# Kernel tuning notes

Hardware: AMD Instinct MI355X
Metric: run time of the kernel (lower is better)

## Reference

```python
import jax, jax.numpy as jnp
import numpy as np

N_TOKEN = 267735
D = 512           # d_embed == d_proj
DIV = 4
CUTS = [0, 20000, 40000, 200000, 267735]  # cutoff_ends
N_TOKENS_BATCH = 1024  # len*bsz


def setup_inputs() -> dict:
    key = jax.random.key(0)
    ks = jax.random.split(key, 16)
    inp = {}
    inp["hidden"] = jax.random.normal(ks[0], (N_TOKENS_BATCH, D), jnp.float32)
    inp["target"] = jax.random.randint(ks[1], (N_TOKENS_BATCH,), 0, N_TOKEN)
    d_embs = [D // DIV ** i for i in range(4)]          # 512, 128, 32, 8
    sizes = [CUTS[i + 1] - CUTS[i] for i in range(4)]   # 20000, 20000, 160000, 67735
    for i in range(4):
        inp[f"W{i}"] = jax.random.normal(ks[2 + 3 * i], (sizes[i], d_embs[i]), jnp.float32) * (d_embs[i] ** -0.5)
        inp[f"b{i}"] = jax.random.normal(ks[3 + 3 * i], (sizes[i],), jnp.float32) * 0.01
        inp[f"proj{i}"] = jax.random.normal(ks[4 + 3 * i], (D, d_embs[i]), jnp.float32) * (D ** -0.5)
    inp["cluster_weight"] = jax.random.normal(ks[14], (3, D), jnp.float32) * (D ** -0.5)
    inp["cluster_bias"] = jax.random.normal(ks[15], (3,), jnp.float32) * 0.01
    return inp


def reference(hidden, target, W0, b0, proj0, W1, b1, proj1, W2, b2, proj2, W3, b3, proj3, cluster_weight, cluster_bias):
    n = jnp.arange(target.shape[0])
    # head = shortlist vocab + one logit per tail cluster
    head_w = jnp.concatenate([W0, cluster_weight], axis=0)   # [20003, D]
    head_b = jnp.concatenate([b0, cluster_bias], axis=0)     # [20003]
    head_logit = (hidden @ proj0) @ head_w.T + head_b        # einsum('bd,de,ev->bv')
    head_lp = jax.nn.log_softmax(head_logit, axis=-1)        # [N, 20003]
    head_size = head_lp.shape[1]
    # cluster id per token (0 = shortlist, 1..3 = tails)
    cid = ((target >= CUTS[1]).astype(jnp.int32)
           + (target >= CUTS[2]).astype(jnp.int32)
           + (target >= CUTS[3]).astype(jnp.int32))
    # shortlist: nll = -head_logprob[n, target]
    nll = -head_lp[n, jnp.clip(target, 0, CUTS[1] - 1)]
    for i, (Wi, bi, pi) in enumerate([(W1, b1, proj1), (W2, b2, proj2), (W3, b3, proj3)], start=1):
        l, r = CUTS[i], CUTS[i + 1]
        tail_lp = jax.nn.log_softmax((hidden @ pi) @ Wi.T + bi, axis=-1)  # [N, r-l]
        rel = jnp.clip(target - l, 0, r - l - 1)
        # faithful to original: head column indexed as head_logprob[:, -i]
        lp_i = head_lp[:, head_size - i] + tail_lp[n, rel]
        nll = jnp.where(cid == i, -lp_i, nll)
    return nll
```

## Files before the change

kernel.cpp:

```cpp
#include <hip/hip_runtime.h>

typedef short s16x8 __attribute__((ext_vector_type(8)));
typedef unsigned short u16x8 __attribute__((ext_vector_type(8)));
typedef float f32x4 __attribute__((ext_vector_type(4)));
typedef unsigned short ushort;

#define NTOK 1024
#define DHID 512

#define VH   20003
#define KH   512
#define NCH_H 80
#define TPC_H 16
#define VH_PAD 20480

#define V1   20000
#define K1   128
#define NCH_1 80
#define TPC_1 16
#define V1_PAD 20480

#define V2   160000
#define K2   32
#define NCH_2 128
#define TPC_2 80
#define V2_PAD 163840

#define V3   67735
#define K3   32
#define NCH_3 67
#define TPC_3 64
#define V3_PAD 68608

#define PAD_BIAS (-1e30f)

#define OFF_HW   0UL
#define OFF_W1   (OFF_HW  + (unsigned long)VH_PAD*KH*2)
#define OFF_W2   (OFF_W1  + (unsigned long)V1_PAD*K1*2)
#define OFF_W3   (OFF_W2  + (unsigned long)V2_PAD*K2*2)
#define OFF_HID  (OFF_W3  + (unsigned long)V3_PAD*K3*2)
#define OFF_PT0  (OFF_HID + (unsigned long)NTOK*DHID*2)
#define OFF_PT1  (OFF_PT0 + (unsigned long)512*DHID*2)
#define OFF_PT2  (OFF_PT1 + (unsigned long)128*DHID*2)
#define OFF_PT3  (OFF_PT2 + (unsigned long)32*DHID*2)
#define OFF_H0   (OFF_PT3 + (unsigned long)32*DHID*2)
#define OFF_H1   (OFF_H0  + (unsigned long)NTOK*512*2)
#define OFF_H2   (OFF_H1  + (unsigned long)NTOK*128*2)
#define OFF_H3   (OFF_H2  + (unsigned long)NTOK*32*2)
#define OFF_HB   (OFF_H3  + (unsigned long)NTOK*32*2)
#define OFF_B1   (OFF_HB  + (unsigned long)VH_PAD*4)
#define OFF_B2   (OFF_B1  + (unsigned long)V1_PAD*4)
#define OFF_B3   (OFF_B2  + (unsigned long)V2_PAD*4)
#define OFF_SH   (OFF_B3  + (unsigned long)V3_PAD*4)
#define OFF_S1   (OFF_SH  + (unsigned long)NTOK*NCH_H*4)
#define OFF_S2   (OFF_S1  + (unsigned long)NTOK*NCH_1*4)
#define OFF_S3   (OFF_S2  + (unsigned long)NTOK*NCH_2*4)

__device__ __forceinline__ ushort f2bf(float f) {
    union { float f; unsigned u; } x; x.f = f;
    unsigned r = x.u + 0x7fffu + ((x.u >> 16) & 1u);
    return (ushort)(r >> 16);
}
__device__ __forceinline__ float bf2f(ushort h) {
    union { unsigned u; float f; } x; x.u = ((unsigned)h) << 16;
    return x.f;
}
__device__ __forceinline__ f32x4 mfma_bf16(s16x8 a, s16x8 b, f32x4 c) {
    return __builtin_amdgcn_mfma_f32_16x16x32_bf16(a, b, c, 0, 0, 0);
}
__device__ __forceinline__ void ld8(const float* p, float* v) {
    float4 a = *(const float4*)p, b = *(const float4*)(p + 4);
    v[0]=a.x; v[1]=a.y; v[2]=a.z; v[3]=a.w; v[4]=b.x; v[5]=b.y; v[6]=b.z; v[7]=b.w;
}

#define WB_HW  20480L
#define WB_W1  5120L
#define WB_W2  10240L
#define WB_W3  4288L
#define WB_HID 1024L
#define WB_PT0 512L
#define WB_PT1 128L
#define WB_PT2 32L
#define WB_PT3 32L
#define WB_TOTAL (WB_HW+WB_W1+WB_W2+WB_W3+WB_HID+WB_PT0+WB_PT1+WB_PT2+WB_PT3)

__global__ __launch_bounds__(256) void prep_wswz(
    const float* __restrict__ hidden,
    const float* __restrict__ W0, const float* __restrict__ cw,
    const float* __restrict__ W1, const float* __restrict__ W2, const float* __restrict__ W3,
    const float* __restrict__ p0, const float* __restrict__ p1,
    const float* __restrict__ p2, const float* __restrict__ p3,
    ushort* __restrict__ hw, ushort* __restrict__ ow1,
    ushort* __restrict__ ow2, ushort* __restrict__ ow3,
    ushort* __restrict__ hid,
    ushort* __restrict__ pT0, ushort* __restrict__ pT1,
    ushort* __restrict__ pT2, ushort* __restrict__ pT3)
{
    int lane = threadIdx.x & 63;
    int r = lane & 15, quad = lane >> 4;
    long wb0 = (long)blockIdx.x * 4 + (threadIdx.x >> 6);
    long nw = (long)gridDim.x * 4;
    for (long wb = wb0; wb < WB_TOTAL; wb += nw) {
        long b = wb;
        float vals[8];
        #pragma unroll
        for (int j = 0; j < 8; ++j) vals[j] = 0.f;
        ushort* dst;
        if (b < WB_HW) {
            long tile = b >> 4, ks = b & 15;
            long v = tile * 16 + r, k = ks * 32 + quad * 8;
            if (v < 20000)      ld8(W0 + v * 512 + k, vals);
            else if (v < VH)    ld8(cw + (v - 20000) * 512 + k, vals);
            dst = hw + b * 512 + (long)lane * 8;
        } else if ((b -= WB_HW) < WB_W1) {
            long tile = b >> 2, ks = b & 3;
            long v = tile * 16 + r, k = ks * 32 + quad * 8;
            if (v < V1) ld8(W1 + v * 128 + k, vals);
            dst = ow1 + b * 512 + (long)lane * 8;
        } else if ((b -= WB_W1) < WB_W2) {
            long v = b * 16 + r;
            if (v < V2) ld8(W2 + v * 32 + quad * 8, vals);
            dst = ow2 + b * 512 + (long)lane * 8;
        } else if ((b -= WB_W2) < WB_W3) {
            long v = b * 16 + r;
            if (v < V3 && quad == 0) ld8(W3 + v * 8, vals);
            dst = ow3 + b * 512 + (long)lane * 8;
        } else if ((b -= WB_W3) < WB_HID) {
            long tile = b >> 4, ks = b & 15;
            long v = tile * 16 + r, k = ks * 32 + quad * 8;
            ld8(hidden + v * 512 + k, vals);
            dst = hid + b * 512 + (long)lane * 8;
        } else if ((b -= WB_HID) < WB_PT0) {
            long tile = b >> 4, ks = b & 15;
            long c = tile * 16 + r, k = ks * 32 + quad * 8;
            #pragma unroll
            for (int j = 0; j < 8; ++j) vals[j] = p0[(k + j) * 512 + c];
            dst = pT0 + b * 512 + (long)lane * 8;
        } else if ((b -= WB_PT0) < WB_PT1) {
            long tile = b >> 4, ks = b & 15;
            long c = tile * 16 + r, k = ks * 32 + quad * 8;
            #pragma unroll
            for (int j = 0; j < 8; ++j) vals[j] = p1[(k + j) * 128 + c];
            dst = pT1 + b * 512 + (long)lane * 8;
        } else if ((b -= WB_PT1) < WB_PT2) {
            long tile = b >> 4, ks = b & 15;
            long c = tile * 16 + r, k = ks * 32 + quad * 8;
            #pragma unroll
            for (int j = 0; j < 8; ++j) vals[j] = p2[(k + j) * 32 + c];
            dst = pT2 + b * 512 + (long)lane * 8;
        } else {
            b -= WB_PT2;
            long tile = b >> 4, ks = b & 15;
            long c = tile * 16 + r, k = ks * 32 + quad * 8;
            if (c < 8) {
                #pragma unroll
                for (int j = 0; j < 8; ++j) vals[j] = p3[(k + j) * 8 + c];
            }
            dst = pT3 + b * 512 + (long)lane * 8;
        }
        u16x8 o;
        #pragma unroll
        for (int j = 0; j < 8; ++j) o[j] = f2bf(vals[j]);
        *(u16x8*)dst = o;
    }
}

#define E_HB  ((long)VH_PAD)
#define E_B1  ((long)V1_PAD)
#define E_B2  ((long)V2_PAD)
#define E_B3  ((long)V3_PAD)
#define E_BIAS (E_HB+E_B1+E_B2+E_B3)

__global__ __launch_bounds__(256) void prep_bias(
    const float* __restrict__ b0, const float* __restrict__ b1,
    const float* __restrict__ b2, const float* __restrict__ b3,
    const float* __restrict__ cb,
    float* __restrict__ hbp, float* __restrict__ ob1,
    float* __restrict__ ob2, float* __restrict__ ob3)
{
    long stride = (long)gridDim.x * blockDim.x;
    for (long i = (long)blockIdx.x * blockDim.x + threadIdx.x; i < E_BIAS; i += stride) {
        long j = i;
        if (j < E_HB) {
            hbp[j] = (j < 20000) ? b0[j] : (j < VH) ? cb[j - 20000] : PAD_BIAS;
        } else if ((j -= E_HB) < E_B1) {
            ob1[j] = (j < V1) ? b1[j] : PAD_BIAS;
        } else if ((j -= E_B1) < E_B2) {
            ob2[j] = (j < V2) ? b2[j] : PAD_BIAS;
        } else { j -= E_B2;
            ob3[j] = (j < V3) ? b3[j] : PAD_BIAS;
        }
    }
}

__global__ __launch_bounds__(256) void gemm_h(
    const ushort* __restrict__ A, const ushort* __restrict__ Bt,
    ushort* __restrict__ Hout, int dpad)
{
    int wave = threadIdx.x >> 6, lane = threadIdx.x & 63;
    int quad = lane >> 4, colid = lane & 15;
    int m_tile = blockIdx.x * 4 + wave;
    int c_tile = blockIdx.y;
    const ushort* Ab = A + ((long)m_tile * 16) * 512 + lane * 8;
    const ushort* Bb = Bt + ((long)c_tile * 16) * 512 + lane * 8;
    f32x4 acc = {0.f, 0.f, 0.f, 0.f};
    #pragma unroll
    for (int ks = 0; ks < 16; ++ks) {
        s16x8 a = *(const s16x8*)(Ab + ks * 512);
        s16x8 b = *(const s16x8*)(Bb + ks * 512);
        acc = mfma_bf16(a, b, acc);
    }
    int KBo = dpad >> 5;
    int col = c_tile * 16 + colid;
    int ks_o = col >> 5, q_o = (col >> 3) & 3, j_o = col & 7;
    #pragma unroll
    for (int r = 0; r < 4; ++r) {
        int rm = quad * 4 + r;
        Hout[((long)m_tile * KBo + ks_o) * 512 + (q_o * 16 + rm) * 8 + j_o] = f2bf(acc[r]);
    }
}

template<int K, int U>
__global__ __launch_bounds__(256, 4) void fused_lse_t(
    const ushort* __restrict__ A, const ushort* __restrict__ W,
    const float* __restrict__ bias, float* __restrict__ part_s,
    int tpc, int n_chunks)
{
    constexpr int KB = K / 32;
    int wave = threadIdx.x >> 6, lane = threadIdx.x & 63;
    int quad = lane >> 4, colid = lane & 15;
    int m_tile = blockIdx.x * 4 + wave;
    int t0 = blockIdx.y * tpc;
    const ushort* Ab = A + ((long)m_tile * KB) * 512 + lane * 8;
    float s_acc[4] = {0.f, 0.f, 0.f, 0.f};

    for (int vt = 0; vt < tpc; vt += U) {
        int tile0 = t0 + vt;
        const ushort* Wb = W + ((long)tile0 * KB) * 512 + lane * 8;
        f32x4 acc[U];
        #pragma unroll
        for (int u = 0; u < U; ++u) acc[u] = (f32x4){0.f, 0.f, 0.f, 0.f};
        #pragma unroll 4
        for (int ks = 0; ks < KB; ++ks) {
            s16x8 a = *(const s16x8*)(Ab + ks * 512);
            #pragma unroll
            for (int u = 0; u < U; ++u) {
                s16x8 b = *(const s16x8*)(Wb + ((long)u * KB + ks) * 512);
                acc[u] = mfma_bf16(a, b, acc[u]);
            }
        }
        #pragma unroll
        for (int u = 0; u < U; ++u) {
            float bval = bias[(tile0 + u) * 16 + colid];
            #pragma unroll
            for (int r = 0; r < 4; ++r)
                s_acc[r] += __expf(acc[u][r] + bval);
        }
    }
    #pragma unroll
    for (int r = 0; r < 4; ++r) {
        float v = s_acc[r];
        v += __shfl_xor(v, 1);
        v += __shfl_xor(v, 2);
        v += __shfl_xor(v, 4);
        v += __shfl_xor(v, 8);
        s_acc[r] = v;
    }
    if (colid == 0) {
        #pragma unroll
        for (int r = 0; r < 4; ++r) {
            int m = m_tile * 16 + quad * 4 + r;
            part_s[(long)m * n_chunks + blockIdx.y] = s_acc[r];
        }
    }
}

__device__ __forceinline__ float swz_dot(const ushort* __restrict__ H, int m,
                                         const ushort* __restrict__ Wm, long vrow,
                                         int K, int lane)
{
    float d = 0.f;
    if (lane * 8 < K) {
        int ks = lane >> 2, q = lane & 3;
        int KB = K >> 5;
        const ushort* hp = H + ((long)(m >> 4) * KB + ks) * 512 + (q * 16 + (m & 15)) * 8;
        const ushort* wp = Wm + ((vrow >> 4) * KB + ks) * 512 + (q * 16 + (int)(vrow & 15)) * 8;
        #pragma unroll
        for (int j = 0; j < 8; ++j) d += bf2f(hp[j]) * bf2f(wp[j]);
    }
    d += __shfl_xor(d, 1);  d += __shfl_xor(d, 2);  d += __shfl_xor(d, 4);
    d += __shfl_xor(d, 8);  d += __shfl_xor(d, 16); d += __shfl_xor(d, 32);
    return d;
}

__global__ __launch_bounds__(256) void finalize_kernel(
    const int* __restrict__ target,
    const ushort* __restrict__ H0, const ushort* __restrict__ hw,
    const float* __restrict__ hbp, const float* __restrict__ sH,
    const ushort* __restrict__ H1, const ushort* __restrict__ w1,
    const float* __restrict__ b1p, const float* __restrict__ s1,
    const ushort* __restrict__ H2, const ushort* __restrict__ w2,
    const float* __restrict__ b2p, const float* __restrict__ s2,
    const ushort* __restrict__ H3, const ushort* __restrict__ w3,
    const float* __restrict__ b3p, const float* __restrict__ s3,
    float* __restrict__ out)
{
    int wave = threadIdx.x >> 6, lane = threadIdx.x & 63;
    int m = blockIdx.x * 4 + wave;
    int t = target[m];
    int cid = (t >= 20000) + (t >= 40000) + (t >= 200000);

    float s = 0.f;
    for (int i = lane; i < NCH_H; i += 64) s += sH[(long)m * NCH_H + i];
    s += __shfl_xor(s, 1);  s += __shfl_xor(s, 2);  s += __shfl_xor(s, 4);
    s += __shfl_xor(s, 8);  s += __shfl_xor(s, 16); s += __shfl_xor(s, 32);
    float lse_h = __logf(s);

    int hc = (cid == 0) ? t : (20003 - cid);
    float d = swz_dot(H0, m, hw, hc, 512, lane);
    float nll = lse_h - (d + hbp[hc]);

    if (cid > 0) {
        const ushort *Hi, *Wi; const float *bi, *si; int K, nc, l;
        if (cid == 1)      { Hi = H1; Wi = w1; bi = b1p; si = s1; K = 128; nc = NCH_1; l = 20000; }
        else if (cid == 2) { Hi = H2; Wi = w2; bi = b2p; si = s2; K = 32;  nc = NCH_2; l = 40000; }
        else               { Hi = H3; Wi = w3; bi = b3p; si = s3; K = 32;  nc = NCH_3; l = 200000; }
        int rel = t - l;
        float ts = 0.f;
        for (int i = lane; i < nc; i += 64) ts += si[(long)m * nc + i];
        ts += __shfl_xor(ts, 1);  ts += __shfl_xor(ts, 2);  ts += __shfl_xor(ts, 4);
        ts += __shfl_xor(ts, 8);  ts += __shfl_xor(ts, 16); ts += __shfl_xor(ts, 32);
        float lse_t = __logf(ts);
        float dt = swz_dot(Hi, m, Wi, rel, K, lane);
        nll += lse_t - (dt + bi[rel]);
    }
    if (lane == 0) out[m] = nll;
}

extern "C" void kernel_launch(void* const* d_in, const int* in_sizes, int n_in,
                              void* d_out, int out_size, void* d_ws, size_t ws_size,
                              hipStream_t stream) {
    const float* hidden = (const float*)d_in[0];
    const int*   target = (const int*)d_in[1];
    const float* W0 = (const float*)d_in[2];
    const float* b0 = (const float*)d_in[3];
    const float* p0 = (const float*)d_in[4];
    const float* W1 = (const float*)d_in[5];
    const float* b1 = (const float*)d_in[6];
    const float* p1 = (const float*)d_in[7];
    const float* W2 = (const float*)d_in[8];
    const float* b2 = (const float*)d_in[9];
    const float* p2 = (const float*)d_in[10];
    const float* W3 = (const float*)d_in[11];
    const float* b3 = (const float*)d_in[12];
    const float* p3 = (const float*)d_in[13];
    const float* cw = (const float*)d_in[14];
    const float* cb = (const float*)d_in[15];

    char* ws = (char*)d_ws;
    ushort* hw  = (ushort*)(ws + OFF_HW);
    ushort* ow1 = (ushort*)(ws + OFF_W1);
    ushort* ow2 = (ushort*)(ws + OFF_W2);
    ushort* ow3 = (ushort*)(ws + OFF_W3);
    ushort* hid = (ushort*)(ws + OFF_HID);
    ushort* pT0 = (ushort*)(ws + OFF_PT0);
    ushort* pT1 = (ushort*)(ws + OFF_PT1);
    ushort* pT2 = (ushort*)(ws + OFF_PT2);
    ushort* pT3 = (ushort*)(ws + OFF_PT3);
    ushort* H0  = (ushort*)(ws + OFF_H0);
    ushort* H1  = (ushort*)(ws + OFF_H1);
    ushort* H2  = (ushort*)(ws + OFF_H2);
    ushort* H3  = (ushort*)(ws + OFF_H3);
    float* hbp = (float*)(ws + OFF_HB);
    float* b1p = (float*)(ws + OFF_B1);
    float* b2p = (float*)(ws + OFF_B2);
    float* b3p = (float*)(ws + OFF_B3);
    float* sH  = (float*)(ws + OFF_SH);
    float* s1  = (float*)(ws + OFF_S1);
    float* s2  = (float*)(ws + OFF_S2);
    float* s3  = (float*)(ws + OFF_S3);

    prep_wswz<<<10464, 256, 0, stream>>>(hidden, W0, cw, W1, W2, W3,
                                         p0, p1, p2, p3,
                                         hw, ow1, ow2, ow3, hid, pT0, pT1, pT2, pT3);
    prep_bias<<<1072, 256, 0, stream>>>(b0, b1, b2, b3, cb, hbp, b1p, b2p, b3p);

    gemm_h<<<dim3(NTOK / 64, 512 / 16), 256, 0, stream>>>(hid, pT0, H0, 512);
    gemm_h<<<dim3(NTOK / 64, 128 / 16), 256, 0, stream>>>(hid, pT1, H1, 128);
    gemm_h<<<dim3(NTOK / 64, 32 / 16),  256, 0, stream>>>(hid, pT2, H2, 32);
    gemm_h<<<dim3(NTOK / 64, 32 / 16),  256, 0, stream>>>(hid, pT3, H3, 32);

    fused_lse_t<KH, 8><<<dim3(NTOK / 64, NCH_H), 256, 0, stream>>>(H0, hw,  hbp, sH, TPC_H, NCH_H);
    fused_lse_t<K1, 8><<<dim3(NTOK / 64, NCH_1), 256, 0, stream>>>(H1, ow1, b1p, s1, TPC_1, NCH_1);
    fused_lse_t<K2, 8><<<dim3(NTOK / 64, NCH_2), 256, 0, stream>>>(H2, ow2, b2p, s2, TPC_2, NCH_2);
    fused_lse_t<K3, 8><<<dim3(NTOK / 64, NCH_3), 256, 0, stream>>>(H3, ow3, b3p, s3, TPC_3, NCH_3);

    finalize_kernel<<<NTOK / 4, 256, 0, stream>>>(target,
        H0, hw, hbp, sH, H1, ow1, b1p, s1, H2, ow2, b2p, s2, H3, ow3, b3p, s3,
        (float*)d_out);
}
```

Baseline: 277.8 us.

## Register-block fused LSE kernel over four row tiles per wave to reuse W loads

The fused log-sum-exp kernel now has each single-wave block compute four 16-row token tiles against the same vocabulary tiles, so each W fragment loaded from memory feeds four MFMAs instead of one. For small K the A fragments are hoisted into registers for the whole chunk. Vocabulary chunk counts are doubled so the grid stays large despite the smaller 64-thread blocks, and the unroll factor drops to 4 for the tail clusters. The cost is higher register pressure, which may lower occupancy, plus twice as many partial sums for finalize to reduce.

```diff
diff --git a/kernel.cpp b/kernel.cpp
--- a/kernel.cpp
+++ b/kernel.cpp
@@ -10,26 +10,26 @@
 
 #define VH   20003
 #define KH   512
-#define NCH_H 80
-#define TPC_H 16
+#define NCH_H 160
+#define TPC_H 8
 #define VH_PAD 20480
 
 #define V1   20000
 #define K1   128
-#define NCH_1 80
-#define TPC_1 16
+#define NCH_1 160
+#define TPC_1 8
 #define V1_PAD 20480
 
 #define V2   160000
 #define K2   32
-#define NCH_2 128
-#define TPC_2 80
+#define NCH_2 256
+#define TPC_2 40
 #define V2_PAD 163840
 
 #define V3   67735
 #define K3   32
-#define NCH_3 67
-#define TPC_3 64
+#define NCH_3 134
+#define TPC_3 32
 #define V3_PAD 68608
 
 #define PAD_BIAS (-1e30f)
@@ -220,58 +220,90 @@
     }
 }
 
-template<int K, int U>
-__global__ __launch_bounds__(256, 4) void fused_lse_t(
+template<int K, int U, int M>
+__global__ __launch_bounds__(64) void fused_lse_t(
     const ushort* __restrict__ A, const ushort* __restrict__ W,
     const float* __restrict__ bias, float* __restrict__ part_s,
     int tpc, int n_chunks)
 {
     constexpr int KB = K / 32;
-    int wave = threadIdx.x >> 6, lane = threadIdx.x & 63;
+    constexpr bool HOIST = (KB <= 4);
+    int lane = threadIdx.x & 63;
     int quad = lane >> 4, colid = lane & 15;
-    int m_tile = blockIdx.x * 4 + wave;
-    int t0 = blockIdx.y * tpc;
-    const ushort* Ab = A + ((long)m_tile * KB) * 512 + lane * 8;
-    float s_acc[4] = {0.f, 0.f, 0.f, 0.f};
+    int mt0 = blockIdx.x * M;
+    int chunk = blockIdx.y;
+    int t0 = chunk * tpc;
+    const ushort* Ab = A + (long)mt0 * KB * 512 + lane * 8;
+
+    float s_acc[M][4];
+    #pragma unroll
+    for (int t = 0; t < M; ++t)
+        #pragma unroll
+        for (int r = 0; r < 4; ++r) s_acc[t][r] = 0.f;
+
+    s16x8 af[M][HOIST ? KB : 1];
+    if constexpr (HOIST) {
+        #pragma unroll
+        for (int t = 0; t < M; ++t)
+            #pragma unroll
+            for (int ks = 0; ks < KB; ++ks)
+                af[t][ks] = *(const s16x8*)(Ab + ((long)t * KB + ks) * 512);
+    }
 
     for (int vt = 0; vt < tpc; vt += U) {
-        int tile0 = t0 + vt;
-        const ushort* Wb = W + ((long)tile0 * KB) * 512 + lane * 8;
-        f32x4 acc[U];
-        #pragma unroll
-        for (int u = 0; u < U; ++u) acc[u] = (f32x4){0.f, 0.f, 0.f, 0.f};
-        #pragma unroll 4
+        const ushort* Wb = W + ((long)(t0 + vt) * KB) * 512 + lane * 8;
+        f32x4 acc[M][U];
+        #pragma unroll
+        for (int t = 0; t < M; ++t)
+            #pragma unroll
+            for (int u = 0; u < U; ++u) acc[t][u] = (f32x4){0.f, 0.f, 0.f, 0.f};
+        #pragma unroll
         for (int ks = 0; ks < KB; ++ks) {
-            s16x8 a = *(const s16x8*)(Ab + ks * 512);
-            #pragma unroll
-            for (int u = 0; u < U; ++u) {
-                s16x8 b = *(const s16x8*)(Wb + ((long)u * KB + ks) * 512);
-                acc[u] = mfma_bf16(a, b, acc[u]);
+            s16x8 b[U];
+            #pragma unroll
+            for (int u = 0; u < U; ++u)
+                b[u] = *(const s16x8*)(Wb + ((long)u * KB + ks) * 512);
+            s16x8 a[M];
+            #pragma unroll
+            for (int t = 0; t < M; ++t) {
+                if constexpr (HOIST) a[t] = af[t][ks];
+                else a[t] = *(const s16x8*)(Ab + ((long)t * KB + ks) * 512);
             }
+            #pragma unroll
+            for (int t = 0; t < M; ++t)
+                #pragma unroll
+                for (int u = 0; u < U; ++u)
+                    acc[t][u] = mfma_bf16(a[t], b[u], acc[t][u]);
         }
         #pragma unroll
         for (int u = 0; u < U; ++u) {
-            float bval = bias[(tile0 + u) * 16 + colid];
-            #pragma unroll
-            for (int r = 0; r < 4; ++r)
-                s_acc[r] += __expf(acc[u][r] + bval);
+            float bval = bias[(t0 + vt + u) * 16 + colid];
+            #pragma unroll
+            for (int t = 0; t < M; ++t)
+                #pragma unroll
+                for (int r = 0; r < 4; ++r)
+                    s_acc[t][r] += __expf(acc[t][u][r] + bval);
         }
     }
     #pragma unroll
-    for (int r = 0; r < 4; ++r) {
-        float v = s_acc[r];
-        v += __shfl_xor(v, 1);
-        v += __shfl_xor(v, 2);
-        v += __shfl_xor(v, 4);
-        v += __shfl_xor(v, 8);
-        s_acc[r] = v;
-    }
+    for (int t = 0; t < M; ++t)
+        #pragma unroll
+        for (int r = 0; r < 4; ++r) {
+            float v = s_acc[t][r];
+            v += __shfl_xor(v, 1);
+            v += __shfl_xor(v, 2);
+            v += __shfl_xor(v, 4);
+            v += __shfl_xor(v, 8);
+            s_acc[t][r] = v;
+        }
     if (colid == 0) {
         #pragma unroll
-        for (int r = 0; r < 4; ++r) {
-            int m = m_tile * 16 + quad * 4 + r;
-            part_s[(long)m * n_chunks + blockIdx.y] = s_acc[r];
-        }
+        for (int t = 0; t < M; ++t)
+            #pragma unroll
+            for (int r = 0; r < 4; ++r) {
+                int m = (mt0 + t) * 16 + quad * 4 + r;
+                part_s[(long)m * n_chunks + chunk] = s_acc[t][r];
+            }
     }
 }
 
@@ -390,10 +422,10 @@
     gemm_h<<<dim3(NTOK / 64, 32 / 16),  256, 0, stream>>>(hid, pT2, H2, 32);
     gemm_h<<<dim3(NTOK / 64, 32 / 16),  256, 0, stream>>>(hid, pT3, H3, 32);
 
-    fused_lse_t<KH, 8><<<dim3(NTOK / 64, NCH_H), 256, 0, stream>>>(H0, hw,  hbp, sH, TPC_H, NCH_H);
-    fused_lse_t<K1, 8><<<dim3(NTOK / 64, NCH_1), 256, 0, stream>>>(H1, ow1, b1p, s1, TPC_1, NCH_1);
-    fused_lse_t<K2, 8><<<dim3(NTOK / 64, NCH_2), 256, 0, stream>>>(H2, ow2, b2p, s2, TPC_2, NCH_2);
-    fused_lse_t<K3, 8><<<dim3(NTOK / 64, NCH_3), 256, 0, stream>>>(H3, ow3, b3p, s3, TPC_3, NCH_3);
+    fused_lse_t<KH, 8, 4><<<dim3(16, NCH_H), 64, 0, stream>>>(H0, hw,  hbp, sH, TPC_H, NCH_H);
+    fused_lse_t<K1, 4, 4><<<dim3(16, NCH_1), 64, 0, stream>>>(H1, ow1, b1p, s1, TPC_1, NCH_1);
+    fused_lse_t<K2, 4, 4><<<dim3(16, NCH_2), 64, 0, stream>>>(H2, ow2, b2p, s2, TPC_2, NCH_2);
+    fused_lse_t<K3, 4, 4><<<dim3(16, NCH_3), 64, 0, stream>>>(H3, ow3, b3p, s3, TPC_3, NCH_3);
 
     finalize_kernel<<<NTOK / 4, 256, 0, stream>>>(target,
         H0, hw, hbp, sH, H1, ow1, b1p, s1, H2, ow2, b2p, s2, H3, ow3, b3p, s3,
```

Result: slower. 372.2 us (+34.0%).

## Stage vocab weight tiles in LDS shared across waves in LSE kernels

Applied to the files above, without the earlier changes.

The fused log-sum-exp kernels now cooperatively load each group of 8 weight tiles into shared memory once per block, and all four waves (each owning a different token tile) read those tiles from LDS. Previously each wave fetched the same weight tiles from global memory on its own. Chunk counts are doubled and tiles per chunk halved to raise grid parallelism. The cost is two barriers per k-slice and LDS pressure, and the occupancy hint was dropped from the launch bounds.

```diff
diff --git a/kernel.cpp b/kernel.cpp
--- a/kernel.cpp
+++ b/kernel.cpp
@@ -10,26 +10,26 @@
 
 #define VH   20003
 #define KH   512
-#define NCH_H 80
-#define TPC_H 16
+#define NCH_H 160
+#define TPC_H 8
 #define VH_PAD 20480
 
 #define V1   20000
 #define K1   128
-#define NCH_1 80
-#define TPC_1 16
+#define NCH_1 160
+#define TPC_1 8
 #define V1_PAD 20480
 
 #define V2   160000
 #define K2   32
-#define NCH_2 128
-#define TPC_2 80
+#define NCH_2 256
+#define TPC_2 40
 #define V2_PAD 163840
 
 #define V3   67735
 #define K3   32
-#define NCH_3 67
-#define TPC_3 64
+#define NCH_3 134
+#define TPC_3 32
 #define V3_PAD 68608
 
 #define PAD_BIAS (-1e30f)
@@ -220,38 +220,52 @@
     }
 }
 
-template<int K, int U>
-__global__ __launch_bounds__(256, 4) void fused_lse_t(
+template<int K, int SKS>
+__global__ __launch_bounds__(256) void fused_lse_lds(
     const ushort* __restrict__ A, const ushort* __restrict__ W,
     const float* __restrict__ bias, float* __restrict__ part_s,
     int tpc, int n_chunks)
 {
     constexpr int KB = K / 32;
+    __shared__ ushort smem[8 * SKS * 512];
+
     int wave = threadIdx.x >> 6, lane = threadIdx.x & 63;
     int quad = lane >> 4, colid = lane & 15;
     int m_tile = blockIdx.x * 4 + wave;
-    int t0 = blockIdx.y * tpc;
-    const ushort* Ab = A + ((long)m_tile * KB) * 512 + lane * 8;
+    int chunk = blockIdx.y;
+    int t0 = chunk * tpc;
+    const ushort* Ab = A + (long)m_tile * KB * 512 + lane * 8;
+
     float s_acc[4] = {0.f, 0.f, 0.f, 0.f};
 
-    for (int vt = 0; vt < tpc; vt += U) {
-        int tile0 = t0 + vt;
-        const ushort* Wb = W + ((long)tile0 * KB) * 512 + lane * 8;
-        f32x4 acc[U];
+    for (int g = 0; g < tpc; g += 8) {
+        f32x4 acc[8];
         #pragma unroll
-        for (int u = 0; u < U; ++u) acc[u] = (f32x4){0.f, 0.f, 0.f, 0.f};
-        #pragma unroll 4
-        for (int ks = 0; ks < KB; ++ks) {
-            s16x8 a = *(const s16x8*)(Ab + ks * 512);
-            #pragma unroll
-            for (int u = 0; u < U; ++u) {
-                s16x8 b = *(const s16x8*)(Wb + ((long)u * KB + ks) * 512);
-                acc[u] = mfma_bf16(a, b, acc[u]);
+        for (int u = 0; u < 8; ++u) acc[u] = (f32x4){0.f, 0.f, 0.f, 0.f};
+
+        for (int kb = 0; kb < KB; kb += SKS) {
+            __syncthreads();
+            #pragma unroll
+            for (int c = 0; c < 2 * SKS; ++c) {
+                int b = wave * 2 * SKS + c;
+                int tile = b / SKS, ksl = b % SKS;
+                u16x8 v = *(const u16x8*)(W + ((long)(t0 + g + tile) * KB + kb + ksl) * 512 + lane * 8);
+                *(u16x8*)(smem + (long)b * 512 + lane * 8) = v;
+            }
+            __syncthreads();
+            #pragma unroll
+            for (int ksl = 0; ksl < SKS; ++ksl) {
+                s16x8 a = *(const s16x8*)(Ab + (long)(kb + ksl) * 512);
+                #pragma unroll
+                for (int u = 0; u < 8; ++u) {
+                    s16x8 b = *(const s16x8*)(smem + (long)(u * SKS + ksl) * 512 + lane * 8);
+                    acc[u] = mfma_bf16(a, b, acc[u]);
+                }
             }
         }
         #pragma unroll
-        for (int u = 0; u < U; ++u) {
-            float bval = bias[(tile0 + u) * 16 + colid];
+        for (int u = 0; u < 8; ++u) {
+            float bval = bias[(t0 + g + u) * 16 + colid];
             #pragma unroll
             for (int r = 0; r < 4; ++r)
                 s_acc[r] += __expf(acc[u][r] + bval);
@@ -264,13 +278,9 @@
         v += __shfl_xor(v, 2);
         v += __shfl_xor(v, 4);
         v += __shfl_xor(v, 8);
-        s_acc[r] = v;
-    }
-    if (colid == 0) {
-        #pragma unroll
-        for (int r = 0; r < 4; ++r) {
+        if (colid == 0) {
             int m = m_tile * 16 + quad * 4 + r;
-            part_s[(long)m * n_chunks + blockIdx.y] = s_acc[r];
+            part_s[(long)m * n_chunks + chunk] = v;
         }
     }
 }
@@ -390,10 +400,10 @@
     gemm_h<<<dim3(NTOK / 64, 32 / 16),  256, 0, stream>>>(hid, pT2, H2, 32);
     gemm_h<<<dim3(NTOK / 64, 32 / 16),  256, 0, stream>>>(hid, pT3, H3, 32);
 
-    fused_lse_t<KH, 8><<<dim3(NTOK / 64, NCH_H), 256, 0, stream>>>(H0, hw,  hbp, sH, TPC_H, NCH_H);
-    fused_lse_t<K1, 8><<<dim3(NTOK / 64, NCH_1), 256, 0, stream>>>(H1, ow1, b1p, s1, TPC_1, NCH_1);
-    fused_lse_t<K2, 8><<<dim3(NTOK / 64, NCH_2), 256, 0, stream>>>(H2, ow2, b2p, s2, TPC_2, NCH_2);
-    fused_lse_t<K3, 8><<<dim3(NTOK / 64, NCH_3), 256, 0, stream>>>(H3, ow3, b3p, s3, TPC_3, NCH_3);
+    fused_lse_lds<KH, 4><<<dim3(16, NCH_H), 256, 0, stream>>>(H0, hw,  hbp, sH, TPC_H, NCH_H);
+    fused_lse_lds<K1, 4><<<dim3(16, NCH_1), 256, 0, stream>>>(H1, ow1, b1p, s1, TPC_1, NCH_1);
+    fused_lse_lds<K2, 1><<<dim3(16, NCH_2), 256, 0, stream>>>(H2, ow2, b2p, s2, TPC_2, NCH_2);
+    fused_lse_lds<K3, 1><<<dim3(16, NCH_3), 256, 0, stream>>>(H3, ow3, b3p, s3, TPC_3, NCH_3);
 
     finalize_kernel<<<NTOK / 4, 256, 0, stream>>>(target,
         H0, hw, hbp, sH, H1, ow1, b1p, s1, H2, ow2, b2p, s2, H3, ow3, b3p, s3,
```

Result: slower. 293.0 us (+5.5%).
